# Performance work log

Measured on AMD Instinct MI355X. Metric: run time of the kernel, lower is better.

The kernel has to match this reference:

```python
import jax, jax.numpy as jnp
import numpy as np
from jax import lax

EPS = 1e-5

def _conv3x3(x, w, b):
    # x: [B,C,H,W], w: [O,I,3,3] -> SAME conv, stride 1
    y = lax.conv_general_dilated(x, w, window_strides=(1, 1), padding='SAME',
                                 dimension_numbers=('NCHW', 'OIHW', 'NCHW'))
    return y + b[None, :, None, None]

def _bn(x, g, be, m, v):
    # inference-mode BatchNorm2d with running stats
    inv = g / jnp.sqrt(v + EPS)
    return x * inv[None, :, None, None] + (be - m * inv)[None, :, None, None]

def _haar_edge(x):
    # pywt.dwt2(x, 'haar') on even H,W reduces to non-overlapping 2x2 blocks:
    #   a=x[2i,2j] b=x[2i,2j+1] c=x[2i+1,2j] d=x[2i+1,2j+1]
    #   LH=(a+b-c-d)/2, HL=(a-b+c-d)/2, HH=(a-b-c+d)/2
    #   edge = LH+HL+HH = (3a - b - c - d)/2
    B, C, H, W = x.shape
    xr = x.reshape(B, C, H // 2, 2, W // 2, 2)
    a = xr[:, :, :, 0, :, 0]
    b = xr[:, :, :, 0, :, 1]
    c = xr[:, :, :, 1, :, 0]
    d = xr[:, :, :, 1, :, 1]
    return (3.0 * a - b - c - d) * 0.5  # [B,C,H//2,W//2]

def reference(x, w1, b1, g1, be1, m1, v1, a_prelu, w2, b2, g2, be2, m2, v2):
    # wavelet edge map, then bilinear upsample to input size (align_corners=False
    # semantics == half-pixel centers, which is jax.image.resize 'bilinear')
    edge = _haar_edge(x)
    edge = jax.image.resize(edge, x.shape, method='bilinear')
    # conv -> BN -> PReLU -> conv -> BN
    h = _bn(_conv3x3(x, w1, b1), g1, be1, m1, v1)
    h = jnp.where(h > 0, h, a_prelu[0] * h)  # PReLU, single shared slope
    h = _bn(_conv3x3(h, w2, b2), g2, be2, m2, v2)
    return x + h + edge

def setup_inputs() -> dict:
    key = jax.random.key(0)
    ks = jax.random.split(key, 4)
    B, C, H, W = 8, 64, 256, 256
    x = jax.random.normal(ks[0], (B, C, H, W), dtype=jnp.float32)
    w1 = jax.random.normal(ks[1], (C, C, 3, 3), dtype=jnp.float32) * 0.05
    w2 = jax.random.normal(ks[2], (C, C, 3, 3), dtype=jnp.float32) * 0.05
    a_prelu = jnp.full((1,), 0.25, dtype=jnp.float32)  # PReLU default init
    zeros = jnp.zeros((C,), dtype=jnp.float32)
    ones = jnp.ones((C,), dtype=jnp.float32)
    return {
        'x': x,
        'w1': w1, 'b1': zeros, 'g1': ones, 'be1': zeros, 'm1': zeros, 'v1': ones,
        'a_prelu': a_prelu,
        'w2': w2, 'b2': zeros, 'g2': ones, 'be2': zeros, 'm2': zeros, 'v2': ones,
    }
```

## Files before the change

kernel.cpp:

```cpp
#include <hip/hip_runtime.h>
#include <cstdint>
#include <cstddef>

typedef __bf16 bf16;
typedef __bf16 bf16x8 __attribute__((ext_vector_type(8)));
typedef __bf16 bf16x4 __attribute__((ext_vector_type(4)));
typedef float  f32x4  __attribute__((ext_vector_type(4)));

#define C_EPS 1e-5f
#define NC_ 64
#define NH_ 256
#define NW_ 256
#define HP_ (NH_*NW_)

#define OFF_W1   0ull
#define OFF_W2   73728ull
#define OFF_AFF  147456ull

__device__ __forceinline__ int lds_off(int p, int cib) {
    return p * 128 + (((cib) ^ (p & 7)) << 4);
}

__global__ void k_pack(const float* __restrict__ w1, const float* __restrict__ w2,
                       const float* __restrict__ b1, const float* __restrict__ g1,
                       const float* __restrict__ be1, const float* __restrict__ m1,
                       const float* __restrict__ v1,
                       const float* __restrict__ b2, const float* __restrict__ g2,
                       const float* __restrict__ be2, const float* __restrict__ m2,
                       const float* __restrict__ v2,
                       bf16* __restrict__ wp1, bf16* __restrict__ wp2,
                       float* __restrict__ aff)
{
    int idx = blockIdx.x * 256 + threadIdx.x;
    if (idx < 2 * 36864) {
        int conv = idx / 36864;
        int u = idx - conv * 36864;
        int j  = u & 7;
        int l  = (u >> 3) & 63;
        int nb = (u >> 9) & 3;
        int kb = (u >> 11) & 1;
        int t  = u >> 12;
        int co = nb * 16 + (l & 15);
        int ci = kb * 32 + ((l >> 4) << 3) + j;
        const float* w = conv ? w2 : w1;
        float val = w[(co * 64 + ci) * 9 + t];
        (conv ? wp2 : wp1)[u] = (bf16)val;
    } else {
        int c = idx - 2 * 36864;
        if (c < 64) {
            float s = g1[c] / sqrtf(v1[c] + C_EPS);
            aff[c]      = s;
            aff[64 + c] = b1[c] * s + (be1[c] - m1[c] * s);
        } else if (c < 128) {
            int cc = c - 64;
            float s = g2[cc] / sqrtf(v2[cc] + C_EPS);
            aff[128 + cc] = s;
            aff[192 + cc] = b2[cc] * s + (be2[cc] - m2[cc] * s);
        }
    }
}

__global__ __launch_bounds__(256, 2)
void k_fused(const float* __restrict__ x, const bf16* __restrict__ wp1,
             const bf16* __restrict__ wp2, const float* __restrict__ aff,
             const float* __restrict__ aprelu, float* __restrict__ out)
{
    __shared__ uint4 smem[4000];
    char* sx = reinterpret_cast<char*>(smem);
    char* se = reinterpret_cast<char*>(smem) + 51200;
    const int t = threadIdx.x;

    const int bid = blockIdx.x;
    const int logical = (bid & 7) * 256 + (bid >> 3);
    const int x0 = (logical & 15) * 16;
    const int y0 = ((logical >> 4) & 15) * 16;
    const int bb = logical >> 8;
    const float* xb = x + (size_t)bb * NC_ * HP_;

    for (int i = 0; i < 25; ++i) {
        int item = i * 256 + t;
        int ci4 = item / 400;
        int p   = item - ci4 * 400;
        int r = p / 20, c = p - r * 20;
        int yy = y0 - 2 + r, xx = x0 - 2 + c;
        float v0 = 0.f, v1 = 0.f, v2 = 0.f, v3 = 0.f;
        if (yy >= 0 && yy < NH_ && xx >= 0 && xx < NW_) {
            const float* s = xb + (size_t)(ci4 * 4) * HP_ + yy * NW_ + xx;
            v0 = s[0]; v1 = s[HP_]; v2 = s[2 * HP_]; v3 = s[3 * HP_];
        }
        bf16x4 pk = { (bf16)v0, (bf16)v1, (bf16)v2, (bf16)v3 };
        *reinterpret_cast<bf16x4*>(sx + lds_off(p, ci4 >> 1) + ((ci4 & 1) << 3)) = pk;
    }
    __syncthreads();

    for (int i = 0; i < 25; ++i) {
        int unit = i * 256 + t;
        int ci = unit & 63;
        int hp = unit >> 6;
        int ry = hp / 10, rx = hp - ry * 10;
        int ryg = (y0 >> 1) - 1 + ry; ryg = ryg < 0 ? 0 : (ryg > 127 ? 127 : ryg);
        int rxg = (x0 >> 1) - 1 + rx; rxg = rxg < 0 ? 0 : (rxg > 127 ? 127 : rxg);
        int pA = (2 * ryg - y0 + 2) * 20 + (2 * rxg - x0 + 2);
        int cib = ci >> 3, cio = (ci & 7) << 1;
        float a  = (float)*reinterpret_cast<const bf16*>(sx + lds_off(pA,      cib) + cio);
        float b_ = (float)*reinterpret_cast<const bf16*>(sx + lds_off(pA + 1,  cib) + cio);
        float c_ = (float)*reinterpret_cast<const bf16*>(sx + lds_off(pA + 20, cib) + cio);
        float d_ = (float)*reinterpret_cast<const bf16*>(sx + lds_off(pA + 21, cib) + cio);
        *reinterpret_cast<bf16*>(se + lds_off(hp, cib) + cio) =
            (bf16)((3.f * a - b_ - c_ - d_) * 0.5f);
    }

    const int w = t >> 6, l = t & 63;
    const int l15 = l & 15, lg = l >> 4;
    f32x4 acc1[6][4];
    #pragma unroll
    for (int j = 0; j < 6; ++j)
        #pragma unroll
        for (int cb = 0; cb < 4; ++cb) acc1[j][cb] = f32x4{0.f, 0.f, 0.f, 0.f};

    int prj[6], pcj[6];
    #pragma unroll
    for (int j = 0; j < 6; ++j) {
        int g = w + 4 * j;
        int p = g * 16 + l15; if (p > 323) p = 323;
        prj[j] = p / 18; pcj[j] = p - prj[j] * 18;
    }

    const bf16x8* wv1 = reinterpret_cast<const bf16x8*>(wp1);
    #pragma unroll
    for (int ky = 0; ky < 3; ++ky)
    #pragma unroll
    for (int kx = 0; kx < 3; ++kx)
    #pragma unroll
    for (int kb = 0; kb < 2; ++kb) {
        const int tap = ky * 3 + kx;
        bf16x8 wf[4];
        #pragma unroll
        for (int cb = 0; cb < 4; ++cb)
            wf[cb] = wv1[(((tap * 2 + kb) * 4 + cb) << 6) + l];
        #pragma unroll
        for (int j = 0; j < 6; ++j) {
            if (w + 4 * j > 20) continue;
            bf16x8 xf = *reinterpret_cast<const bf16x8*>(
                sx + lds_off((prj[j] + ky) * 20 + pcj[j] + kx, kb * 4 + lg));
            #pragma unroll
            for (int cb = 0; cb < 4; ++cb)
                acc1[j][cb] = __builtin_amdgcn_mfma_f32_16x16x32_bf16(wf[cb], xf, acc1[j][cb], 0, 0, 0);
        }
    }
    __syncthreads();

    {
        const float apv = aprelu[0];
        #pragma unroll
        for (int j = 0; j < 6; ++j) {
            int g = w + 4 * j;
            if (g > 20) continue;
            int p = g * 16 + l15;
            if (p < 324) {
                const int hy = y0 - 1 + prj[j];
                const int hx = x0 - 1 + pcj[j];
                const bool valid = (hy >= 0) && (hy < NH_) && (hx >= 0) && (hx < NW_);
                #pragma unroll
                for (int cb = 0; cb < 4; ++cb) {
                    f32x4 al = *reinterpret_cast<const f32x4*>(aff + cb * 16 + lg * 4);
                    f32x4 be = *reinterpret_cast<const f32x4*>(aff + 64 + cb * 16 + lg * 4);
                    bf16x4 pk;
                    #pragma unroll
                    for (int r = 0; r < 4; ++r) {
                        float zv = acc1[j][cb][r] * al[r] + be[r];
                        float hv = zv > 0.f ? zv : apv * zv;
                        pk[r] = valid ? (bf16)hv : (bf16)0.f;
                    }
                    *reinterpret_cast<bf16x4*>(sx + lds_off(p, cb * 2 + (lg >> 1)) + ((lg & 1) << 3)) = pk;
                }
            }
        }
    }
    __syncthreads();

    f32x4 acc2[4][4];
    #pragma unroll
    for (int a = 0; a < 4; ++a)
        #pragma unroll
        for (int b = 0; b < 4; ++b) acc2[a][b] = f32x4{0.f, 0.f, 0.f, 0.f};

    const bf16x8* wv2 = reinterpret_cast<const bf16x8*>(wp2);
    #pragma unroll
    for (int ky = 0; ky < 3; ++ky)
    #pragma unroll
    for (int kx = 0; kx < 3; ++kx)
    #pragma unroll
    for (int kb = 0; kb < 2; ++kb) {
        const int tap = ky * 3 + kx;
        bf16x8 wf[4];
        #pragma unroll
        for (int cb = 0; cb < 4; ++cb)
            wf[cb] = wv2[(((tap * 2 + kb) * 4 + cb) << 6) + l];
        #pragma unroll
        for (int pr = 0; pr < 4; ++pr) {
            int p = (w * 4 + pr + ky) * 18 + (l15 + kx);
            bf16x8 xf = *reinterpret_cast<const bf16x8*>(sx + lds_off(p, kb * 4 + lg));
            #pragma unroll
            for (int cb = 0; cb < 4; ++cb)
                acc2[pr][cb] = __builtin_amdgcn_mfma_f32_16x16x32_bf16(xf, wf[cb], acc2[pr][cb], 0, 0, 0);
        }
    }

    #pragma unroll
    for (int cb = 0; cb < 4; ++cb) {
        const int co = cb * 16 + l15;
        const int cib2 = co >> 3;
        const int cio = (co & 7) << 1;
        float et[4][4];
        #pragma unroll
        for (int r = 0; r < 4; ++r)
            #pragma unroll
            for (int c = 0; c < 4; ++c) {
                int ep = (2 * w + r) * 10 + (2 * lg + c);
                et[r][c] = (float)*reinterpret_cast<const bf16*>(se + lds_off(ep, cib2) + cio);
            }
        const float al = aff[128 + co];
        const float bt = aff[192 + co];
        const float* xs0 = x + ((size_t)bb * NC_ + co) * HP_;
        #pragma unroll
        for (int pr = 0; pr < 4; ++pr) {
            const int Y = y0 + w * 4 + pr;
            const int Xb = x0 + lg * 4;
            const int ry0 = (pr == 0) ? 0 : (pr == 3 ? 2 : 1);
            const float wyl = (pr & 1) ? 0.75f : 0.25f;
            f32x4 xq = *reinterpret_cast<const f32x4*>(xs0 + Y * NW_ + Xb);
            f32x4 o;
            #pragma unroll
            for (int rr = 0; rr < 4; ++rr) {
                const int rx0 = (rr == 0) ? 0 : (rr == 3 ? 2 : 1);
                const float wxl = (rr & 1) ? 0.75f : 0.25f;
                float e0 = wxl * et[ry0][rx0]     + (1.f - wxl) * et[ry0][rx0 + 1];
                float e1 = wxl * et[ry0 + 1][rx0] + (1.f - wxl) * et[ry0 + 1][rx0 + 1];
                float e  = wyl * e0 + (1.f - wyl) * e1;
                o[rr] = acc2[pr][cb][rr] * al + bt + xq[rr] + e;
            }
            float* os = out + ((size_t)bb * NC_ + co) * HP_ + Y * NW_ + Xb;
            *reinterpret_cast<f32x4*>(os) = o;
        }
    }
}

extern "C" void kernel_launch(void* const* d_in, const int* in_sizes, int n_in,
                              void* d_out, int out_size, void* d_ws, size_t ws_size,
                              hipStream_t stream)
{
    const float* x   = (const float*)d_in[0];
    const float* w1  = (const float*)d_in[1];
    const float* b1  = (const float*)d_in[2];
    const float* g1  = (const float*)d_in[3];
    const float* be1 = (const float*)d_in[4];
    const float* m1  = (const float*)d_in[5];
    const float* v1  = (const float*)d_in[6];
    const float* ap  = (const float*)d_in[7];
    const float* w2  = (const float*)d_in[8];
    const float* b2  = (const float*)d_in[9];
    const float* g2  = (const float*)d_in[10];
    const float* be2 = (const float*)d_in[11];
    const float* m2  = (const float*)d_in[12];
    const float* v2  = (const float*)d_in[13];

    char* ws = (char*)d_ws;
    bf16*  wp1  = (bf16*)(ws + OFF_W1);
    bf16*  wp2  = (bf16*)(ws + OFF_W2);
    float* aff  = (float*)(ws + OFF_AFF);
    float* outp = (float*)d_out;

    k_pack<<<dim3(290), dim3(256), 0, stream>>>(w1, w2, b1, g1, be1, m1, v1,
                                                b2, g2, be2, m2, v2, wp1, wp2, aff);
    k_fused<<<dim3(2048), dim3(256), 0, stream>>>(x, wp1, wp2, aff, ap, outp);
}
```

Measured before the change: 186.3 us.

## Compute Haar edge from global x in epilogue to free LDS for occupancy

Drops the LDS-staged Haar edge tile and its separate compute pass. The epilogue now computes each edge value directly from fp32 global x with clamped float2 loads. This shrinks shared memory from about 64KB to 51KB and raises the launch bound target to 3 blocks per CU, aiming for more occupancy. In exchange it adds many scattered global (likely cache-hit) loads in the epilogue, and it also changes edge precision from bf16-staged to fp32.

```diff
diff --git a/kernel.cpp b/kernel.cpp
--- a/kernel.cpp
+++ b/kernel.cpp
@@ -60,14 +60,13 @@
     }
 }
 
-__global__ __launch_bounds__(256, 2)
+__global__ __launch_bounds__(256, 3)
 void k_fused(const float* __restrict__ x, const bf16* __restrict__ wp1,
              const bf16* __restrict__ wp2, const float* __restrict__ aff,
              const float* __restrict__ aprelu, float* __restrict__ out)
 {
-    __shared__ uint4 smem[4000];
+    __shared__ uint4 smem[3200];
     char* sx = reinterpret_cast<char*>(smem);
-    char* se = reinterpret_cast<char*>(smem) + 51200;
     const int t = threadIdx.x;
 
     const int bid = blockIdx.x;
@@ -93,25 +92,9 @@
     }
     __syncthreads();
 
-    for (int i = 0; i < 25; ++i) {
-        int unit = i * 256 + t;
-        int ci = unit & 63;
-        int hp = unit >> 6;
-        int ry = hp / 10, rx = hp - ry * 10;
-        int ryg = (y0 >> 1) - 1 + ry; ryg = ryg < 0 ? 0 : (ryg > 127 ? 127 : ryg);
-        int rxg = (x0 >> 1) - 1 + rx; rxg = rxg < 0 ? 0 : (rxg > 127 ? 127 : rxg);
-        int pA = (2 * ryg - y0 + 2) * 20 + (2 * rxg - x0 + 2);
-        int cib = ci >> 3, cio = (ci & 7) << 1;
-        float a  = (float)*reinterpret_cast<const bf16*>(sx + lds_off(pA,      cib) + cio);
-        float b_ = (float)*reinterpret_cast<const bf16*>(sx + lds_off(pA + 1,  cib) + cio);
-        float c_ = (float)*reinterpret_cast<const bf16*>(sx + lds_off(pA + 20, cib) + cio);
-        float d_ = (float)*reinterpret_cast<const bf16*>(sx + lds_off(pA + 21, cib) + cio);
-        *reinterpret_cast<bf16*>(se + lds_off(hp, cib) + cio) =
-            (bf16)((3.f * a - b_ - c_ - d_) * 0.5f);
-    }
-
     const int w = t >> 6, l = t & 63;
     const int l15 = l & 15, lg = l >> 4;
+
     f32x4 acc1[6][4];
     #pragma unroll
     for (int j = 0; j < 6; ++j)
@@ -210,19 +193,24 @@
     #pragma unroll
     for (int cb = 0; cb < 4; ++cb) {
         const int co = cb * 16 + l15;
-        const int cib2 = co >> 3;
-        const int cio = (co & 7) << 1;
+        const float* xs0 = x + ((size_t)bb * NC_ + co) * HP_;
         float et[4][4];
         #pragma unroll
-        for (int r = 0; r < 4; ++r)
+        for (int r = 0; r < 4; ++r) {
+            int gry = (y0 >> 1) - 1 + 2 * w + r;
+            gry = gry < 0 ? 0 : (gry > 127 ? 127 : gry);
+            const float* row0 = xs0 + (size_t)(2 * gry) * NW_;
             #pragma unroll
             for (int c = 0; c < 4; ++c) {
-                int ep = (2 * w + r) * 10 + (2 * lg + c);
-                et[r][c] = (float)*reinterpret_cast<const bf16*>(se + lds_off(ep, cib2) + cio);
+                int grx = (x0 >> 1) - 1 + 2 * lg + c;
+                grx = grx < 0 ? 0 : (grx > 127 ? 127 : grx);
+                float2 A = *reinterpret_cast<const float2*>(row0 + 2 * grx);
+                float2 B = *reinterpret_cast<const float2*>(row0 + NW_ + 2 * grx);
+                et[r][c] = (3.f * A.x - A.y - B.x - B.y) * 0.5f;
             }
+        }
         const float al = aff[128 + co];
         const float bt = aff[192 + co];
-        const float* xs0 = x + ((size_t)bb * NC_ + co) * HP_;
         #pragma unroll
         for (int pr = 0; pr < 4; ++pr) {
             const int Y = y0 + w * 4 + pr;
```

Measured after the change: 326.9 us. 75.5% more time.

## Precompute NHWC bf16 input and Haar edge map in a separate prep kernel

Applied to the files above, without the earlier changes.

Adds a k_prep kernel that transposes x from NCHW fp32 to NHWC bf16 in workspace and computes the Haar edge map once. The fused kernel then loads its halo tile with 16-byte vector loads instead of strided scalar fp32 gathers, and no longer computes the edge per tile. This removes redundant halo and edge work and the uncoalesced channel-strided loads. In exchange there is an extra launch and an extra round trip to global memory of about 80 MB.

```diff
diff --git a/kernel.cpp b/kernel.cpp
--- a/kernel.cpp
+++ b/kernel.cpp
@@ -13,12 +13,14 @@
 #define NW_ 256
 #define HP_ (NH_*NW_)
 
-#define OFF_W1   0ull
-#define OFF_W2   73728ull
-#define OFF_AFF  147456ull
-
-__device__ __forceinline__ int lds_off(int p, int cib) {
-    return p * 128 + (((cib) ^ (p & 7)) << 4);
+#define OFF_XH   0ull
+#define OFF_EDGE 67108864ull
+#define OFF_W1   83886080ull
+#define OFF_W2   83959808ull
+#define OFF_AFF  84033536ull
+
+__device__ __forceinline__ int lds_off(int p, int g) {
+    return p * 128 + (((g) ^ (p & 7)) << 4);
 }
 
 __global__ void k_pack(const float* __restrict__ w1, const float* __restrict__ w2,
@@ -61,7 +63,51 @@
 }
 
 __global__ __launch_bounds__(256, 2)
-void k_fused(const float* __restrict__ x, const bf16* __restrict__ wp1,
+void k_prep(const float* __restrict__ x, bf16* __restrict__ xh,
+            bf16* __restrict__ edge)
+{
+    __shared__ uint4 smem[4096];
+    char* sr = reinterpret_cast<char*>(smem);
+    const int t = threadIdx.x;
+    const int Y = blockIdx.x & 127;
+    const int b = blockIdx.x >> 7;
+    const float* xb = x + (size_t)b * NC_ * HP_;
+
+    for (int i = 0; i < 128; ++i) {
+        int r  = i >> 6, ci = i & 63;
+        float v = xb[(size_t)ci * HP_ + (2 * Y + r) * NW_ + t];
+        int pp = r * 256 + t;
+        *reinterpret_cast<bf16*>(sr + lds_off(pp, ci >> 3) + ((ci & 7) << 1)) = (bf16)v;
+    }
+    __syncthreads();
+
+    bf16* xhb = xh + ((size_t)b * NH_ + 2 * Y) * NW_ * 64;
+    for (int i = 0; i < 16; ++i) {
+        int u = i * 256 + t;
+        int pp = u >> 3, g = u & 7;
+        uint4 v = *reinterpret_cast<const uint4*>(sr + lds_off(pp, g));
+        *reinterpret_cast<uint4*>(xhb + (size_t)pp * 64 + g * 8) = v;
+    }
+
+    bf16* eb = edge + ((size_t)b * 128 + Y) * 128 * 64;
+    for (int i = 0; i < 4; ++i) {
+        int u = i * 256 + t;
+        int ex = u >> 3, g = u & 7;
+        bf16x8 a  = *reinterpret_cast<const bf16x8*>(sr + lds_off(2 * ex, g));
+        bf16x8 bb = *reinterpret_cast<const bf16x8*>(sr + lds_off(2 * ex + 1, g));
+        bf16x8 c  = *reinterpret_cast<const bf16x8*>(sr + lds_off(256 + 2 * ex, g));
+        bf16x8 d  = *reinterpret_cast<const bf16x8*>(sr + lds_off(256 + 2 * ex + 1, g));
+        bf16x8 e;
+        #pragma unroll
+        for (int j = 0; j < 8; ++j)
+            e[j] = (bf16)((3.f * (float)a[j] - (float)bb[j] - (float)c[j] - (float)d[j]) * 0.5f);
+        *reinterpret_cast<bf16x8*>(eb + (size_t)ex * 64 + g * 8) = e;
+    }
+}
+
+__global__ __launch_bounds__(256, 2)
+void k_fused(const float* __restrict__ x, const bf16* __restrict__ xh,
+             const bf16* __restrict__ edge, const bf16* __restrict__ wp1,
              const bf16* __restrict__ wp2, const float* __restrict__ aff,
              const float* __restrict__ aprelu, float* __restrict__ out)
 {
@@ -75,43 +121,37 @@
     const int x0 = (logical & 15) * 16;
     const int y0 = ((logical >> 4) & 15) * 16;
     const int bb = logical >> 8;
-    const float* xb = x + (size_t)bb * NC_ * HP_;
-
-    for (int i = 0; i < 25; ++i) {
-        int item = i * 256 + t;
-        int ci4 = item / 400;
-        int p   = item - ci4 * 400;
-        int r = p / 20, c = p - r * 20;
-        int yy = y0 - 2 + r, xx = x0 - 2 + c;
-        float v0 = 0.f, v1 = 0.f, v2 = 0.f, v3 = 0.f;
-        if (yy >= 0 && yy < NH_ && xx >= 0 && xx < NW_) {
-            const float* s = xb + (size_t)(ci4 * 4) * HP_ + yy * NW_ + xx;
-            v0 = s[0]; v1 = s[HP_]; v2 = s[2 * HP_]; v3 = s[3 * HP_];
-        }
-        bf16x4 pk = { (bf16)v0, (bf16)v1, (bf16)v2, (bf16)v3 };
-        *reinterpret_cast<bf16x4*>(sx + lds_off(p, ci4 >> 1) + ((ci4 & 1) << 3)) = pk;
+
+    const bf16* xhb = xh + (size_t)bb * NH_ * NW_ * 64;
+    for (int i = 0; i < 13; ++i) {
+        int u = i * 256 + t;
+        if (u < 3200) {
+            int p = u >> 3, g = u & 7;
+            int r = p / 20, c = p - r * 20;
+            int yy = y0 - 2 + r, xx = x0 - 2 + c;
+            uint4 v = {0u, 0u, 0u, 0u};
+            if (yy >= 0 && yy < NH_ && xx >= 0 && xx < NW_)
+                v = *reinterpret_cast<const uint4*>(xhb + ((size_t)(yy * NW_ + xx)) * 64 + g * 8);
+            *reinterpret_cast<uint4*>(sx + lds_off(p, g)) = v;
+        }
+    }
+    const bf16* eb = edge + (size_t)bb * 128 * 128 * 64;
+    for (int i = 0; i < 4; ++i) {
+        int u = i * 256 + t;
+        if (u < 800) {
+            int p = u >> 3, g = u & 7;
+            int ry = p / 10, rx = p - ry * 10;
+            int ryg = (y0 >> 1) - 1 + ry; ryg = ryg < 0 ? 0 : (ryg > 127 ? 127 : ryg);
+            int rxg = (x0 >> 1) - 1 + rx; rxg = rxg < 0 ? 0 : (rxg > 127 ? 127 : rxg);
+            uint4 v = *reinterpret_cast<const uint4*>(eb + ((size_t)(ryg * 128 + rxg)) * 64 + g * 8);
+            *reinterpret_cast<uint4*>(se + lds_off(p, g)) = v;
+        }
     }
     __syncthreads();
-
-    for (int i = 0; i < 25; ++i) {
-        int unit = i * 256 + t;
-        int ci = unit & 63;
-        int hp = unit >> 6;
-        int ry = hp / 10, rx = hp - ry * 10;
-        int ryg = (y0 >> 1) - 1 + ry; ryg = ryg < 0 ? 0 : (ryg > 127 ? 127 : ryg);
-        int rxg = (x0 >> 1) - 1 + rx; rxg = rxg < 0 ? 0 : (rxg > 127 ? 127 : rxg);
-        int pA = (2 * ryg - y0 + 2) * 20 + (2 * rxg - x0 + 2);
-        int cib = ci >> 3, cio = (ci & 7) << 1;
-        float a  = (float)*reinterpret_cast<const bf16*>(sx + lds_off(pA,      cib) + cio);
-        float b_ = (float)*reinterpret_cast<const bf16*>(sx + lds_off(pA + 1,  cib) + cio);
-        float c_ = (float)*reinterpret_cast<const bf16*>(sx + lds_off(pA + 20, cib) + cio);
-        float d_ = (float)*reinterpret_cast<const bf16*>(sx + lds_off(pA + 21, cib) + cio);
-        *reinterpret_cast<bf16*>(se + lds_off(hp, cib) + cio) =
-            (bf16)((3.f * a - b_ - c_ - d_) * 0.5f);
-    }
 
     const int w = t >> 6, l = t & 63;
     const int l15 = l & 15, lg = l >> 4;
+
     f32x4 acc1[6][4];
     #pragma unroll
     for (int j = 0; j < 6; ++j)
@@ -266,6 +306,8 @@
     const float* v2  = (const float*)d_in[13];
 
     char* ws = (char*)d_ws;
+    bf16*  xhb  = (bf16*)(ws + OFF_XH);
+    bf16*  ebuf = (bf16*)(ws + OFF_EDGE);
     bf16*  wp1  = (bf16*)(ws + OFF_W1);
     bf16*  wp2  = (bf16*)(ws + OFF_W2);
     float* aff  = (float*)(ws + OFF_AFF);
@@ -273,5 +315,6 @@
 
     k_pack<<<dim3(290), dim3(256), 0, stream>>>(w1, w2, b1, g1, be1, m1, v1,
                                                 b2, g2, be2, m2, v2, wp1, wp2, aff);
-    k_fused<<<dim3(2048), dim3(256), 0, stream>>>(x, wp1, wp2, aff, ap, outp);
-}
+    k_prep<<<dim3(1024), dim3(256), 0, stream>>>(x, xhb, ebuf);
+    k_fused<<<dim3(2048), dim3(256), 0, stream>>>(x, xhb, ebuf, wp1, wp2, aff, ap, outp);
+}
```

New measurement: 230.5 us. 23.7% more time.
